# Optimization experiments

Measured on AMD Instinct MI355X. Metric: run time of the kernel, lower is better.

## Reference

```python
import jax, jax.numpy as jnp
import numpy as np
import math

N_STATIONS = 50  # N in [N, 7, 56] causal matrix


def setup_inputs() -> dict:
    key = jax.random.key(0)
    k1, k2, k3, k4 = jax.random.split(key, 4)
    B, L, H, E = 3200, 7, 8, 64
    S, D = 56, 64
    queries = jax.random.normal(k1, (B, L, H, E), dtype=jnp.float32)
    keys = jax.random.normal(k2, (B, S, H, E), dtype=jnp.float32)
    values = jax.random.normal(k3, (B, S, H, D), dtype=jnp.float32)
    # station-specific multiplicative causal matrix in [0, 1]
    attn_mask = jax.random.uniform(k4, (N_STATIONS, L, S), dtype=jnp.float32)
    return {"queries": queries, "keys": keys, "values": values, "attn_mask": attn_mask}


def reference(queries, keys, values, attn_mask):
    B, L, H, E = queries.shape
    S = values.shape[1]
    N = attn_mask.shape[0]  # number of stations; B % N == 0
    ab = B // N  # actual batch size per station group
    scale = 1.0 / math.sqrt(E)
    # raw scores [B, H, L, S]
    scores = jnp.einsum('blhe,bshe->bhls', queries, keys)
    # multiplicative station-specific mask: reshape batch into (ab, N) and
    # broadcast mask [N, L, S] over (ab, H)
    masked = scores.reshape(ab, N, H, L, S) * attn_mask[None, :, None, :, :]
    masked = masked.reshape(B, H, L, S)
    # note: scale is applied AFTER masking, as in the original module
    A = jax.nn.softmax(scale * masked, axis=-1)  # dropout is identity at eval
    V = jnp.einsum('bhls,bshd->blhd', A, values)
    return V
```

## Files before the change

kernel.cpp:

```cpp
#include <hip/hip_runtime.h>
#include <math.h>


typedef __attribute__((ext_vector_type(8))) _Float16 half8;

__launch_bounds__(512)
__global__ void fullattn_kernel(const float* __restrict__ q,
                                const float* __restrict__ k,
                                const float* __restrict__ v,
                                const float* __restrict__ mask,
                                float* __restrict__ out,
                                int nstations) {
    __shared__ __align__(16) _Float16 KL8[8][56 * 64];

    const int lane = threadIdx.x & 63;
    const int wid  = __builtin_amdgcn_readfirstlane(threadIdx.x >> 6);
    const int b    = blockIdx.x;
    const int h    = wid;
    const int st   = b % nstations;

    _Float16* KL = KL8[wid];

    const int kbase = b * 28672 + h * 64;
    const int qbase = b * 3584  + h * 64;

    const int ml = (lane < 56) ? lane : 55;
    float m[7];
#pragma unroll
    for (int l = 0; l < 7; ++l)
        m[l] = mask[st * 392 + l * 56 + ml] * 0.125f;

#pragma unroll
    for (int i = 0; i < 7; ++i) {
        const int f = i * 64 + lane;
        const int s = f >> 3;
        const int c = f & 7;
        const float4 a0 = *(const float4*)(k + kbase + s * 512 + c * 8);
        const float4 a1 = *(const float4*)(k + kbase + s * 512 + c * 8 + 4);
        half8 hv;
        hv[0] = (_Float16)a0.x; hv[1] = (_Float16)a0.y;
        hv[2] = (_Float16)a0.z; hv[3] = (_Float16)a0.w;
        hv[4] = (_Float16)a1.x; hv[5] = (_Float16)a1.y;
        hv[6] = (_Float16)a1.z; hv[7] = (_Float16)a1.w;
        *(half8*)(&KL[s * 64 + 8 * (c ^ (s & 7))]) = hv;
    }

    const int sr = (lane < 56) ? lane : 55;
    const int sx = sr & 7;
    const float* qp = q + qbase;

    float acc[7];
#pragma unroll
    for (int l = 0; l < 7; ++l) acc[l] = 0.0f;

#pragma unroll
    for (int c = 0; c < 8; ++c) {
        const half8 kv = *(const half8*)(&KL[sr * 64 + 8 * (c ^ sx)]);
        float kf[8];
#pragma unroll
        for (int j = 0; j < 8; ++j) kf[j] = (float)kv[j];
#pragma unroll
        for (int l = 0; l < 7; ++l) {
            const float4 q0 = *(const float4*)(qp + l * 512 + c * 8);
            const float4 q1 = *(const float4*)(qp + l * 512 + c * 8 + 4);
            acc[l] = fmaf(q0.x, kf[0], acc[l]);
            acc[l] = fmaf(q0.y, kf[1], acc[l]);
            acc[l] = fmaf(q0.z, kf[2], acc[l]);
            acc[l] = fmaf(q0.w, kf[3], acc[l]);
            acc[l] = fmaf(q1.x, kf[4], acc[l]);
            acc[l] = fmaf(q1.y, kf[5], acc[l]);
            acc[l] = fmaf(q1.z, kf[6], acc[l]);
            acc[l] = fmaf(q1.w, kf[7], acc[l]);
        }
    }

    float vb0[28];
#pragma unroll
    for (int i = 0; i < 28; ++i) vb0[i] = v[kbase + i * 512 + lane];

    float* pbuf = (float*)KL;
    float rdenom[7];
#pragma unroll
    for (int l = 0; l < 7; ++l) {
        const float sc = acc[l] * m[l];
        const float p  = (lane < 56) ? __expf(sc) : 0.0f;
        float sum = p;
#pragma unroll
        for (int off = 32; off >= 1; off >>= 1)
            sum += __shfl_xor(sum, off);
        pbuf[l * 64 + lane] = p;
        rdenom[l] = __builtin_amdgcn_rcpf(sum);
    }

    float vb1[28];
#pragma unroll
    for (int i = 0; i < 28; ++i) vb1[i] = v[kbase + (28 + i) * 512 + lane];

    float facc[7];
#pragma unroll
    for (int l = 0; l < 7; ++l) facc[l] = 0.0f;

#pragma unroll
    for (int s4 = 0; s4 < 7; ++s4) {
#pragma unroll
        for (int l = 0; l < 7; ++l) {
            const float4 p4 = *(const float4*)(&pbuf[l * 64 + s4 * 4]);
            facc[l] = fmaf(p4.x, vb0[s4 * 4 + 0], facc[l]);
            facc[l] = fmaf(p4.y, vb0[s4 * 4 + 1], facc[l]);
            facc[l] = fmaf(p4.z, vb0[s4 * 4 + 2], facc[l]);
            facc[l] = fmaf(p4.w, vb0[s4 * 4 + 3], facc[l]);
        }
    }
#pragma unroll
    for (int s4 = 0; s4 < 7; ++s4) {
#pragma unroll
        for (int l = 0; l < 7; ++l) {
            const float4 p4 = *(const float4*)(&pbuf[l * 64 + 28 + s4 * 4]);
            facc[l] = fmaf(p4.x, vb1[s4 * 4 + 0], facc[l]);
            facc[l] = fmaf(p4.y, vb1[s4 * 4 + 1], facc[l]);
            facc[l] = fmaf(p4.z, vb1[s4 * 4 + 2], facc[l]);
            facc[l] = fmaf(p4.w, vb1[s4 * 4 + 3], facc[l]);
        }
    }

#pragma unroll
    for (int l = 0; l < 7; ++l)
        out[qbase + l * 512 + lane] = facc[l] * rdenom[l];
}

extern "C" void kernel_launch(void* const* d_in, const int* in_sizes, int n_in,
                              void* d_out, int out_size, void* d_ws, size_t ws_size,
                              hipStream_t stream) {
    const float* q    = (const float*)d_in[0];
    const float* k    = (const float*)d_in[1];
    const float* v    = (const float*)d_in[2];
    const float* mask = (const float*)d_in[3];
    float* out        = (float*)d_out;

    const int B = in_sizes[0] / (7 * 8 * 64);
    const int nstations = in_sizes[3] / (7 * 56);

    fullattn_kernel<<<dim3(B), dim3(512), 0, stream>>>(q, k, v, mask, out, nstations);
}
```

Baseline: 196.3 us.

## Stage K and V cooperatively in shared fp16 with fully coalesced block loads

K is now loaded by the whole block as contiguous 32-byte chunks covering all heads and written to a shared fp16 buffer, instead of each wave gathering only its own head's strided rows. V is also staged through the same shared buffer in fp16, with part of it prefetched into registers early to overlap with QK, and the probabilities are stored in fp16 shared memory. This cuts register pressure (launch bounds now ask for 4 blocks per CU) and improves load coalescing. The cost is block-wide barriers and extra fp16 rounding of V and P.

```diff
diff --git a/kernel.cpp b/kernel.cpp
--- a/kernel.cpp
+++ b/kernel.cpp
@@ -4,61 +4,76 @@
 
 typedef __attribute__((ext_vector_type(8))) _Float16 half8;
 
-__launch_bounds__(512)
+static __device__ __forceinline__ half8 cvt8(const float4 a, const float4 b) {
+    half8 h;
+    h[0] = (_Float16)a.x; h[1] = (_Float16)a.y;
+    h[2] = (_Float16)a.z; h[3] = (_Float16)a.w;
+    h[4] = (_Float16)b.x; h[5] = (_Float16)b.y;
+    h[6] = (_Float16)b.z; h[7] = (_Float16)b.w;
+    return h;
+}
+
+__launch_bounds__(512, 4)
 __global__ void fullattn_kernel(const float* __restrict__ q,
                                 const float* __restrict__ k,
                                 const float* __restrict__ v,
                                 const float* __restrict__ mask,
                                 float* __restrict__ out,
                                 int nstations) {
-    __shared__ __align__(16) _Float16 KL8[8][56 * 64];
+    __shared__ __align__(16) _Float16 KV[28672];
+    __shared__ __align__(16) _Float16 P[8 * 7 * 64];
 
-    const int lane = threadIdx.x & 63;
-    const int wid  = __builtin_amdgcn_readfirstlane(threadIdx.x >> 6);
+    const int t    = threadIdx.x;
+    const int lane = t & 63;
+    const int w    = __builtin_amdgcn_readfirstlane(t >> 6);
     const int b    = blockIdx.x;
-    const int h    = wid;
     const int st   = b % nstations;
 
-    _Float16* KL = KL8[wid];
+    const int kb = b * 28672;
+    const int qb = b * 3584;
 
-    const int kbase = b * 28672 + h * 64;
-    const int qbase = b * 3584  + h * 64;
+    {
+        const float* kp = k + kb + t * 8;
+        const int hh = lane >> 3;
+        const int c  = t & 7;
+#pragma unroll
+        for (int i = 0; i < 7; ++i) {
+            const float4 a0 = *(const float4*)(kp + i * 4096);
+            const float4 a1 = *(const float4*)(kp + i * 4096 + 4);
+            const int s = i * 8 + w;
+            *(half8*)(&KV[s * 512 + hh * 64 + ((c ^ (s & 7)) << 3)]) = cvt8(a0, a1);
+        }
+    }
+    float4 vp[8];
+    {
+        const float* vpg = v + kb + t * 8;
+#pragma unroll
+        for (int i = 0; i < 4; ++i) {
+            vp[2 * i]     = *(const float4*)(vpg + i * 4096);
+            vp[2 * i + 1] = *(const float4*)(vpg + i * 4096 + 4);
+        }
+    }
+    __syncthreads();
 
-    const int ml = (lane < 56) ? lane : 55;
+    const int ml  = (lane < 56) ? lane : 55;
+    const int sxr = ml & 7;
+
     float m[7];
 #pragma unroll
     for (int l = 0; l < 7; ++l)
         m[l] = mask[st * 392 + l * 56 + ml] * 0.125f;
 
-#pragma unroll
-    for (int i = 0; i < 7; ++i) {
-        const int f = i * 64 + lane;
-        const int s = f >> 3;
-        const int c = f & 7;
-        const float4 a0 = *(const float4*)(k + kbase + s * 512 + c * 8);
-        const float4 a1 = *(const float4*)(k + kbase + s * 512 + c * 8 + 4);
-        half8 hv;
-        hv[0] = (_Float16)a0.x; hv[1] = (_Float16)a0.y;
-        hv[2] = (_Float16)a0.z; hv[3] = (_Float16)a0.w;
-        hv[4] = (_Float16)a1.x; hv[5] = (_Float16)a1.y;
-        hv[6] = (_Float16)a1.z; hv[7] = (_Float16)a1.w;
-        *(half8*)(&KL[s * 64 + 8 * (c ^ (s & 7))]) = hv;
-    }
-
-    const int sr = (lane < 56) ? lane : 55;
-    const int sx = sr & 7;
-    const float* qp = q + qbase;
-
+    const float* qp = q + qb + w * 64;
     float acc[7];
 #pragma unroll
     for (int l = 0; l < 7; ++l) acc[l] = 0.0f;
 
 #pragma unroll
     for (int c = 0; c < 8; ++c) {
-        const half8 kv = *(const half8*)(&KL[sr * 64 + 8 * (c ^ sx)]);
+        const half8 kv8 = *(const half8*)(&KV[ml * 512 + w * 64 + ((c ^ sxr) << 3)]);
         float kf[8];
 #pragma unroll
-        for (int j = 0; j < 8; ++j) kf[j] = (float)kv[j];
+        for (int j = 0; j < 8; ++j) kf[j] = (float)kv8[j];
 #pragma unroll
         for (int l = 0; l < 7; ++l) {
             const float4 q0 = *(const float4*)(qp + l * 512 + c * 8);
@@ -74,11 +89,6 @@
         }
     }
 
-    float vb0[28];
-#pragma unroll
-    for (int i = 0; i < 28; ++i) vb0[i] = v[kbase + i * 512 + lane];
-
-    float* pbuf = (float*)KL;
     float rdenom[7];
 #pragma unroll
     for (int l = 0; l < 7; ++l) {
@@ -88,44 +98,53 @@
 #pragma unroll
         for (int off = 32; off >= 1; off >>= 1)
             sum += __shfl_xor(sum, off);
-        pbuf[l * 64 + lane] = p;
+        P[w * 448 + l * 64 + lane] = (_Float16)p;
         rdenom[l] = __builtin_amdgcn_rcpf(sum);
     }
+    __syncthreads();
 
-    float vb1[28];
+    {
 #pragma unroll
-    for (int i = 0; i < 28; ++i) vb1[i] = v[kbase + (28 + i) * 512 + lane];
+        for (int i = 0; i < 4; ++i)
+            *(half8*)(&KV[i * 4096 + t * 8]) = cvt8(vp[2 * i], vp[2 * i + 1]);
+        const float* vpg = v + kb + t * 8;
+#pragma unroll
+        for (int i = 4; i < 7; ++i) {
+            const float4 a0 = *(const float4*)(vpg + i * 4096);
+            const float4 a1 = *(const float4*)(vpg + i * 4096 + 4);
+            *(half8*)(&KV[i * 4096 + t * 8]) = cvt8(a0, a1);
+        }
+    }
+    __syncthreads();
 
     float facc[7];
 #pragma unroll
     for (int l = 0; l < 7; ++l) facc[l] = 0.0f;
 
+    const int vbase = w * 64 + lane;
 #pragma unroll
-    for (int s4 = 0; s4 < 7; ++s4) {
+    for (int sc8 = 0; sc8 < 7; ++sc8) {
+        float vv[8];
+#pragma unroll
+        for (int j = 0; j < 8; ++j)
+            vv[j] = (float)KV[(sc8 * 8 + j) * 512 + vbase];
 #pragma unroll
         for (int l = 0; l < 7; ++l) {
-            const float4 p4 = *(const float4*)(&pbuf[l * 64 + s4 * 4]);
-            facc[l] = fmaf(p4.x, vb0[s4 * 4 + 0], facc[l]);
-            facc[l] = fmaf(p4.y, vb0[s4 * 4 + 1], facc[l]);
-            facc[l] = fmaf(p4.z, vb0[s4 * 4 + 2], facc[l]);
-            facc[l] = fmaf(p4.w, vb0[s4 * 4 + 3], facc[l]);
-        }
-    }
-#pragma unroll
-    for (int s4 = 0; s4 < 7; ++s4) {
-#pragma unroll
-        for (int l = 0; l < 7; ++l) {
-            const float4 p4 = *(const float4*)(&pbuf[l * 64 + 28 + s4 * 4]);
-            facc[l] = fmaf(p4.x, vb1[s4 * 4 + 0], facc[l]);
-            facc[l] = fmaf(p4.y, vb1[s4 * 4 + 1], facc[l]);
-            facc[l] = fmaf(p4.z, vb1[s4 * 4 + 2], facc[l]);
-            facc[l] = fmaf(p4.w, vb1[s4 * 4 + 3], facc[l]);
+            const half8 p8 = *(const half8*)(&P[w * 448 + l * 64 + sc8 * 8]);
+            facc[l] = fmaf((float)p8[0], vv[0], facc[l]);
+            facc[l] = fmaf((float)p8[1], vv[1], facc[l]);
+            facc[l] = fmaf((float)p8[2], vv[2], facc[l]);
+            facc[l] = fmaf((float)p8[3], vv[3], facc[l]);
+            facc[l] = fmaf((float)p8[4], vv[4], facc[l]);
+            facc[l] = fmaf((float)p8[5], vv[5], facc[l]);
+            facc[l] = fmaf((float)p8[6], vv[6], facc[l]);
+            facc[l] = fmaf((float)p8[7], vv[7], facc[l]);
         }
     }
 
 #pragma unroll
     for (int l = 0; l < 7; ++l)
-        out[qbase + l * 512 + lane] = facc[l] * rdenom[l];
+        out[qb + l * 512 + vbase] = facc[l] * rdenom[l];
 }
 
 extern "C" void kernel_launch(void* const* d_in, const int* in_sizes, int n_in,
```

Measured after the change: 215.3 us. +9.7%, slower.
